# Kernel tuning notes

Hardware: AMD Instinct MI355X
Metric: run time of the kernel (lower is better)

## Reference

```python
import jax, jax.numpy as jnp
import numpy as np

B, IN, OUT = 2048, 512, 512

def setup_inputs() -> dict:
    key = jax.random.key(0)
    k1, k2, k3 = jax.random.split(key, 3)
    x = jax.random.normal(k1, (B, IN), dtype=jnp.float32)
    dilation_weight = jax.random.normal(k2, (OUT, IN), dtype=jnp.float32)
    erosion_weight = jax.random.normal(k3, (OUT, IN), dtype=jnp.float32)
    return {"x": x, "dilation_weight": dilation_weight, "erosion_weight": erosion_weight}

def reference(x, dilation_weight, erosion_weight):
    # tropical (max-plus) matmul: [B,1,IN] + [OUT,IN] -> max over IN -> [B,OUT]
    dilation = jnp.max(x[:, None, :] + dilation_weight, axis=2)
    # (min-minus): [B,1,IN] - [OUT,IN] -> min over IN -> [B,OUT]
    erosion = jnp.min(x[:, None, :] - erosion_weight, axis=2)
    return dilation + erosion
```

## Files before the change

kernel.cpp:

```cpp
#include <hip/hip_runtime.h>
#include <math.h>

#define B_TOT 2048
#define IN_TOT 512
#define OUT_TOT 512
#define CPB 8
#define RPB 128
#define M 4
#define NQ 128

__global__ __launch_bounds__(256, 4) void morph_kernel(
    const float* __restrict__ x,
    const float* __restrict__ wdil,
    const float* __restrict__ wero,
    float* __restrict__ out)
{
    __shared__ float w_s[2][CPB * IN_TOT];

    const int tid = (int)threadIdx.x;
    const int tx  = tid & 7;
    const int ty  = tid >> 3;

    const int col0 = (int)blockIdx.x * CPB;
    const int row0 = (int)blockIdx.y * RPB;

#pragma unroll
    for (int i = 0; i < 4; ++i) {
        const int s  = i * 256 + tid;
        const int c  = s >> 7;
        const int qp = s & 127;
        const int ql = (qp & ~7) | ((qp ^ c) & 7);
        const int g  = (col0 + c) * IN_TOT + ql * 4;
        *(float4*)&w_s[0][s * 4] = *(const float4*)(wdil + g);
        *(float4*)&w_s[1][s * 4] = *(const float4*)(wero + g);
    }
    __syncthreads();

    float dil[M], ero[M];
#pragma unroll
    for (int mi = 0; mi < M; ++mi) { dil[mi] = -INFINITY; ero[mi] = INFINITY; }

    const float* xr = x + (size_t)(row0 + ty) * IN_TOT;

    const float* __restrict__ wdp = &w_s[0][tx * IN_TOT];
    const float* __restrict__ wep = &w_s[1][tx * IN_TOT];

#pragma unroll 4
    for (int q = 0; q < NQ; ++q) {
        const int ph = (q & ~7) | ((q ^ tx) & 7);
        float4 wd4 = *(const float4*)(wdp + ph * 4);
        float4 we4 = *(const float4*)(wep + ph * 4);

        float4 xv[M];
#pragma unroll
        for (int mi = 0; mi < M; ++mi)
            xv[mi] = *(const float4*)(xr + (size_t)(32 * mi) * IN_TOT + q * 4);

#pragma unroll
        for (int mi = 0; mi < M; ++mi) {
            dil[mi] = fmaxf(fmaxf(xv[mi].x + wd4.x, xv[mi].y + wd4.y), dil[mi]);
            dil[mi] = fmaxf(fmaxf(xv[mi].z + wd4.z, xv[mi].w + wd4.w), dil[mi]);
            ero[mi] = fminf(fminf(xv[mi].x - we4.x, xv[mi].y - we4.y), ero[mi]);
            ero[mi] = fminf(fminf(xv[mi].z - we4.z, xv[mi].w - we4.w), ero[mi]);
        }
    }

    float* op = out + (size_t)(row0 + ty) * OUT_TOT + col0 + tx;
#pragma unroll
    for (int mi = 0; mi < M; ++mi)
        op[(size_t)32 * mi * OUT_TOT] = dil[mi] + ero[mi];
}

extern "C" void kernel_launch(void* const* d_in, const int* in_sizes, int n_in,
                              void* d_out, int out_size, void* d_ws, size_t ws_size,
                              hipStream_t stream)
{
    const float* x  = (const float*)d_in[0];
    const float* wd = (const float*)d_in[1];
    const float* we = (const float*)d_in[2];
    float* out = (float*)d_out;

    dim3 grid(OUT_TOT / CPB, B_TOT / RPB);
    dim3 block(256);
    hipLaunchKernelGGL(morph_kernel, grid, block, 0, stream, x, wd, we, out);
}
```

Before: 67.42 us.

## Split reduction dimension across two thread halves with rows-per-block doubled

Doubles the block to 512 threads. Each half reduces over half of the IN dimension, and the partial max/min results are combined through shared memory before the store. Each thread now handles 8 rows instead of 4, so each shared-memory weight load is reused across more x rows, and the grid has half as many blocks. In exchange it raises register pressure, needs an extra shared-memory combine with two barriers, and halves the number of blocks (1024 total).

Result: slower. 226.4 us (+235.7%).

```diff
diff --git a/kernel.cpp b/kernel.cpp
--- a/kernel.cpp
+++ b/kernel.cpp
@@ -5,34 +5,36 @@
 #define IN_TOT 512
 #define OUT_TOT 512
 #define CPB 8
-#define RPB 128
-#define M 4
-#define NQ 128
+#define RPB 256
+#define M 8
+#define QH 64
 
-__global__ __launch_bounds__(256, 4) void morph_kernel(
+__global__ __launch_bounds__(512, 4) void morph_kernel(
     const float* __restrict__ x,
     const float* __restrict__ wdil,
     const float* __restrict__ wero,
     float* __restrict__ out)
 {
-    __shared__ float w_s[2][CPB * IN_TOT];
+    __shared__ float w_s[2 * CPB * IN_TOT / 1];
 
-    const int tid = (int)threadIdx.x;
-    const int tx  = tid & 7;
-    const int ty  = tid >> 3;
+    const int tid  = (int)threadIdx.x;
+    const int half = tid >> 8;
+    const int t    = tid & 255;
+    const int tx   = t & 7;
+    const int ty   = t >> 3;
 
     const int col0 = (int)blockIdx.x * CPB;
     const int row0 = (int)blockIdx.y * RPB;
 
 #pragma unroll
-    for (int i = 0; i < 4; ++i) {
-        const int s  = i * 256 + tid;
+    for (int i = 0; i < 2; ++i) {
+        const int s  = i * 512 + tid;
         const int c  = s >> 7;
         const int qp = s & 127;
         const int ql = (qp & ~7) | ((qp ^ c) & 7);
         const int g  = (col0 + c) * IN_TOT + ql * 4;
-        *(float4*)&w_s[0][s * 4] = *(const float4*)(wdil + g);
-        *(float4*)&w_s[1][s * 4] = *(const float4*)(wero + g);
+        *(float4*)&w_s[s * 4]        = *(const float4*)(wdil + g);
+        *(float4*)&w_s[4096 + s * 4] = *(const float4*)(wero + g);
     }
     __syncthreads();
 
@@ -40,35 +42,57 @@
 #pragma unroll
     for (int mi = 0; mi < M; ++mi) { dil[mi] = -INFINITY; ero[mi] = INFINITY; }
 
-    const float* xr = x + (size_t)(row0 + ty) * IN_TOT;
+    const float* xr[M];
+#pragma unroll
+    for (int mi = 0; mi < M; ++mi)
+        xr[mi] = x + (size_t)(row0 + ty + 32 * mi) * IN_TOT + half * (QH * 4);
 
-    const float* __restrict__ wdp = &w_s[0][tx * IN_TOT];
-    const float* __restrict__ wep = &w_s[1][tx * IN_TOT];
+    const float* __restrict__ wdp = &w_s[tx * 512];
+    const float* __restrict__ wep = &w_s[4096 + tx * 512];
 
-#pragma unroll 4
-    for (int q = 0; q < NQ; ++q) {
-        const int ph = (q & ~7) | ((q ^ tx) & 7);
-        float4 wd4 = *(const float4*)(wdp + ph * 4);
-        float4 we4 = *(const float4*)(wep + ph * 4);
+#pragma unroll 1
+    for (int g = 0; g < QH / 8; ++g) {
+#pragma unroll
+        for (int u = 0; u < 8; ++u) {
+            const int qq = g * 8 + u;
+            const int q  = half * QH + qq;
+            const int ph = (q & ~7) | ((q ^ tx) & 7);
+            float4 wd4 = *(const float4*)(wdp + ph * 4);
+            float4 we4 = *(const float4*)(wep + ph * 4);
 
-        float4 xv[M];
+            float4 xv[M];
 #pragma unroll
-        for (int mi = 0; mi < M; ++mi)
-            xv[mi] = *(const float4*)(xr + (size_t)(32 * mi) * IN_TOT + q * 4);
+            for (int mi = 0; mi < M; ++mi)
+                xv[mi] = *(const float4*)(xr[mi] + qq * 4);
 
 #pragma unroll
-        for (int mi = 0; mi < M; ++mi) {
-            dil[mi] = fmaxf(fmaxf(xv[mi].x + wd4.x, xv[mi].y + wd4.y), dil[mi]);
-            dil[mi] = fmaxf(fmaxf(xv[mi].z + wd4.z, xv[mi].w + wd4.w), dil[mi]);
-            ero[mi] = fminf(fminf(xv[mi].x - we4.x, xv[mi].y - we4.y), ero[mi]);
-            ero[mi] = fminf(fminf(xv[mi].z - we4.z, xv[mi].w - we4.w), ero[mi]);
+            for (int mi = 0; mi < M; ++mi) {
+                dil[mi] = fmaxf(fmaxf(xv[mi].x + wd4.x, xv[mi].y + wd4.y), dil[mi]);
+                dil[mi] = fmaxf(fmaxf(xv[mi].z + wd4.z, xv[mi].w + wd4.w), dil[mi]);
+                ero[mi] = fminf(fminf(xv[mi].x - we4.x, xv[mi].y - we4.y), ero[mi]);
+                ero[mi] = fminf(fminf(xv[mi].z - we4.z, xv[mi].w - we4.w), ero[mi]);
+            }
         }
     }
 
-    float* op = out + (size_t)(row0 + ty) * OUT_TOT + col0 + tx;
+    __syncthreads();
+    if (half == 1) {
 #pragma unroll
-    for (int mi = 0; mi < M; ++mi)
-        op[(size_t)32 * mi * OUT_TOT] = dil[mi] + ero[mi];
+        for (int mi = 0; mi < M; ++mi) {
+            w_s[mi * 256 + t]        = dil[mi];
+            w_s[2048 + mi * 256 + t] = ero[mi];
+        }
+    }
+    __syncthreads();
+    if (half == 0) {
+        float* op = out + (size_t)(row0 + ty) * OUT_TOT + col0 + tx;
+#pragma unroll
+        for (int mi = 0; mi < M; ++mi) {
+            float d = fmaxf(dil[mi], w_s[mi * 256 + t]);
+            float e = fminf(ero[mi], w_s[2048 + mi * 256 + t]);
+            op[(size_t)32 * mi * OUT_TOT] = d + e;
+        }
+    }
 }
 
 extern "C" void kernel_launch(void* const* d_in, const int* in_sizes, int n_in,
@@ -81,6 +105,6 @@
     float* out = (float*)d_out;
 
     dim3 grid(OUT_TOT / CPB, B_TOT / RPB);
-    dim3 block(256);
+    dim3 block(512);
     hipLaunchKernelGGL(morph_kernel, grid, block, 0, stream, x, wd, we, out);
 }
```

## Software-pipeline x and weight loads with a four-stage register prefetch ring

Applied to the files above, without the earlier changes.

Restructures the inner reduction loop into a manually pipelined ring of four register buffers. Global loads of x and LDS loads of the weights for step q+4 are issued right after computing step q, so memory latency overlaps with the max/min arithmetic. Launch bounds are relaxed from 4 to 2 blocks per CU so the compiler can hold the extra prefetch registers, which may reduce occupancy. The last iterations re-load clamped indices, a small amount of redundant traffic.

New measurement: 117.5 us. +74.2%, slower.

```diff
diff --git a/kernel.cpp b/kernel.cpp
--- a/kernel.cpp
+++ b/kernel.cpp
@@ -9,13 +9,13 @@
 #define M 4
 #define NQ 128
 
-__global__ __launch_bounds__(256, 4) void morph_kernel(
+__global__ __launch_bounds__(256, 2) void morph_kernel(
     const float* __restrict__ x,
     const float* __restrict__ wdil,
     const float* __restrict__ wero,
     float* __restrict__ out)
 {
-    __shared__ float w_s[2][CPB * IN_TOT];
+    __shared__ float w_s[2 * CPB * IN_TOT];
 
     const int tid = (int)threadIdx.x;
     const int tx  = tid & 7;
@@ -31,8 +31,8 @@
         const int qp = s & 127;
         const int ql = (qp & ~7) | ((qp ^ c) & 7);
         const int g  = (col0 + c) * IN_TOT + ql * 4;
-        *(float4*)&w_s[0][s * 4] = *(const float4*)(wdil + g);
-        *(float4*)&w_s[1][s * 4] = *(const float4*)(wero + g);
+        *(float4*)&w_s[s * 4]        = *(const float4*)(wdil + g);
+        *(float4*)&w_s[4096 + s * 4] = *(const float4*)(wero + g);
     }
     __syncthreads();
 
@@ -40,30 +40,60 @@
 #pragma unroll
     for (int mi = 0; mi < M; ++mi) { dil[mi] = -INFINITY; ero[mi] = INFINITY; }
 
-    const float* xr = x + (size_t)(row0 + ty) * IN_TOT;
+    const float* xr0 = x + (size_t)(row0 + ty) * IN_TOT;
+    const float* xr1 = xr0 + (size_t)32 * IN_TOT;
+    const float* xr2 = xr0 + (size_t)64 * IN_TOT;
+    const float* xr3 = xr0 + (size_t)96 * IN_TOT;
 
-    const float* __restrict__ wdp = &w_s[0][tx * IN_TOT];
-    const float* __restrict__ wep = &w_s[1][tx * IN_TOT];
+    const float* __restrict__ wdp = &w_s[tx * 512];
+    const float* __restrict__ wep = &w_s[4096 + tx * 512];
 
-#pragma unroll 4
-    for (int q = 0; q < NQ; ++q) {
-        const int ph = (q & ~7) | ((q ^ tx) & 7);
-        float4 wd4 = *(const float4*)(wdp + ph * 4);
-        float4 we4 = *(const float4*)(wep + ph * 4);
+#define XISSUE(b, qq) do { const int _o = (qq) * 4;          \
+        b[0] = *(const float4*)(xr0 + _o);                   \
+        b[1] = *(const float4*)(xr1 + _o);                   \
+        b[2] = *(const float4*)(xr2 + _o);                   \
+        b[3] = *(const float4*)(xr3 + _o); } while (0)
 
-        float4 xv[M];
-#pragma unroll
-        for (int mi = 0; mi < M; ++mi)
-            xv[mi] = *(const float4*)(xr + (size_t)(32 * mi) * IN_TOT + q * 4);
+#define WISSUE(wdv, wev, qq) do {                            \
+        const int _p = ((((qq) & ~7) | (((qq) ^ tx) & 7)) << 2); \
+        wdv = *(const float4*)(wdp + _p);                    \
+        wev = *(const float4*)(wep + _p); } while (0)
 
-#pragma unroll
-        for (int mi = 0; mi < M; ++mi) {
-            dil[mi] = fmaxf(fmaxf(xv[mi].x + wd4.x, xv[mi].y + wd4.y), dil[mi]);
-            dil[mi] = fmaxf(fmaxf(xv[mi].z + wd4.z, xv[mi].w + wd4.w), dil[mi]);
-            ero[mi] = fminf(fminf(xv[mi].x - we4.x, xv[mi].y - we4.y), ero[mi]);
-            ero[mi] = fminf(fminf(xv[mi].z - we4.z, xv[mi].w - we4.w), ero[mi]);
-        }
+#define COMPUTE(xb, wd4, we4) do {                           \
+        _Pragma("unroll")                                    \
+        for (int mi = 0; mi < M; ++mi) {                     \
+            dil[mi] = fmaxf(fmaxf(xb[mi].x + wd4.x, xb[mi].y + wd4.y), dil[mi]); \
+            dil[mi] = fmaxf(fmaxf(xb[mi].z + wd4.z, xb[mi].w + wd4.w), dil[mi]); \
+            ero[mi] = fminf(fminf(xb[mi].x - we4.x, xb[mi].y - we4.y), ero[mi]); \
+            ero[mi] = fminf(fminf(xb[mi].z - we4.z, xb[mi].w - we4.w), ero[mi]); \
+        } } while (0)
+
+    float4 x0[M], x1[M], x2[M], x3[M];
+    float4 wd0, we0, wd1, we1, wd2, we2, wd3, we3;
+
+    XISSUE(x0, 0); XISSUE(x1, 1); XISSUE(x2, 2); XISSUE(x3, 3);
+    WISSUE(wd0, we0, 0); WISSUE(wd1, we1, 1);
+    WISSUE(wd2, we2, 2); WISSUE(wd3, we3, 3);
+
+#pragma unroll 1
+    for (int q = 0; q < NQ; q += 4) {
+        int qn = q + 4; if (qn > NQ - 4) qn = NQ - 4;
+
+        COMPUTE(x0, wd0, we0);
+        XISSUE(x0, qn);     WISSUE(wd0, we0, qn);
+
+        COMPUTE(x1, wd1, we1);
+        XISSUE(x1, qn + 1); WISSUE(wd1, we1, qn + 1);
+
+        COMPUTE(x2, wd2, we2);
+        XISSUE(x2, qn + 2); WISSUE(wd2, we2, qn + 2);
+
+        COMPUTE(x3, wd3, we3);
+        XISSUE(x3, qn + 3); WISSUE(wd3, we3, qn + 3);
     }
+#undef XISSUE
+#undef WISSUE
+#undef COMPUTE
 
     float* op = out + (size_t)(row0 + ty) * OUT_TOT + col0 + tx;
 #pragma unroll
```
